# Performance work log

Measured on AMD Instinct MI355X. Metric: run time of the kernel, lower is better.

## Reference

```python
import jax, jax.numpy as jnp
import numpy as np
from jax import lax

B, C, H, W = 32, 512, 32, 32
NH = 8
ER = 4
DK_RATIO = 0.2
EPS_LN = 1e-6


def _layernorm(t, g, b):
    m = t.mean(-1, keepdims=True)
    v = ((t - m) ** 2).mean(-1, keepdims=True)
    return (t - m) / jnp.sqrt(v + EPS_LN) * g + b


def setup_inputs() -> dict:
    key = jax.random.key(0)
    ks = jax.random.split(key, 24)
    s = 0.02
    dh = C // NH
    return {
        "x": jax.random.normal(ks[0], (B, C, H, W), jnp.float32),
        "mask_u": jax.random.uniform(ks[1], (B, NH, dh, dh), jnp.float32),
        "dw_w": jax.random.normal(ks[2], (C, 1, 3, 3), jnp.float32) * s,
        "dw_b": jnp.zeros((C,), jnp.float32),
        "ln1_g": jnp.ones((C,), jnp.float32),
        "ln1_b": jnp.zeros((C,), jnp.float32),
        "qkv_w": jax.random.normal(ks[3], (3 * C, C), jnp.float32) * s,
        "qkv_b": jnp.zeros((3 * C,), jnp.float32),
        "temp": jnp.ones((NH, 1, 1), jnp.float32),
        "proj_w": jax.random.normal(ks[4], (C, C), jnp.float32) * s,
        "proj_b": jnp.zeros((C,), jnp.float32),
        "ct_w": jax.random.normal(ks[5], (C, C, 2, 2), jnp.float32) * s,  # [in,out,kH,kW]
        "ct_b": jnp.zeros((C,), jnp.float32),
        "ln2_g": jnp.ones((C,), jnp.float32),
        "ln2_b": jnp.zeros((C,), jnp.float32),
        "pw1_w": jax.random.normal(ks[6], (ER * C, C), jnp.float32) * s,
        "pw1_b": jnp.zeros((ER * C,), jnp.float32),
        "pw2_w": jax.random.normal(ks[7], (C, ER * C), jnp.float32) * s,
        "pw2_b": jnp.zeros((C,), jnp.float32),
    }


def reference(x, mask_u, dw_w, dw_b, ln1_g, ln1_b, qkv_w, qkv_b, temp,
              proj_w, proj_b, ct_w, ct_b, ln2_g, ln2_b,
              pw1_w, pw1_b, pw2_w, pw2_b):
    inp = x
    b, c, h, w = x.shape
    # depthwise 3x3 conv + residual
    dw = lax.conv_general_dilated(
        x, dw_w, (1, 1), "SAME", feature_group_count=c,
        dimension_numbers=("NCHW", "OIHW", "NCHW")) + dw_b[None, :, None, None]
    x = dw + inp
    # 2x2 avg pool, stride 2
    hp, wp = h // 2, w // 2
    x = x.reshape(b, c, hp, 2, wp, 2).mean(axis=(3, 5))  # [B,C,hp,wp]
    n = hp * wp
    # tokens [B,N,C] -> LN -> qkv
    t = x.reshape(b, c, n).transpose(0, 2, 1)
    t = _layernorm(t, ln1_g, ln1_b)
    qkv = t @ qkv_w.T + qkv_b                       # [B,N,3C]
    dh = c // NH
    qkv = qkv.reshape(b, n, 3, NH, dh).transpose(2, 0, 3, 1, 4)  # [3,B,h,N,d]
    # cosine (XCA-style) attention: transpose to [B,h,d,N], normalize over N
    q = jnp.swapaxes(qkv[0], -2, -1)
    k = jnp.swapaxes(qkv[1], -2, -1)
    v = jnp.swapaxes(qkv[2], -2, -1)
    q = q / jnp.maximum(jnp.linalg.norm(q, axis=-1, keepdims=True), 1e-12)
    k = k / jnp.maximum(jnp.linalg.norm(k, axis=-1, keepdims=True), 1e-12)
    attn = jnp.einsum("bhdn,bhen->bhde", q, k) * temp  # [B,h,d,d]
    attn = attn + (mask_u < DK_RATIO).astype(attn.dtype) * (-1e12)
    attn = jax.nn.softmax(attn, axis=-1)
    out = jnp.einsum("bhde,bhen->bhdn", attn, v)       # [B,h,d,N]
    out = out.transpose(0, 3, 1, 2).reshape(b, n, c)
    t = out @ proj_w.T + proj_b
    t = t + t
    x = t.transpose(0, 2, 1).reshape(b, c, hp, wp)
    # ConvTranspose2d(C,C,2,stride=2): each pixel expands to 2x2 block
    x = jnp.einsum("bchw,copq->bohpwq", x, ct_w).reshape(b, c, 2 * hp, 2 * wp)
    x = x + ct_b[None, :, None, None]
    # MLP in channels-last
    y = x.transpose(0, 2, 3, 1)                        # [B,H,W,C]
    y = _layernorm(y, ln2_g, ln2_b)
    y = jax.nn.gelu(y @ pw1_w.T + pw1_b, approximate=False)
    y = y @ pw2_w.T + pw2_b
    x = y.transpose(0, 3, 1, 2)
    return inp + x
```

## Files before the change

### kernel.cpp

```cpp
#include <hip/hip_runtime.h>
#include <hip/hip_bf16.h>
#include <math.h>

typedef unsigned short ushort;
typedef __attribute__((ext_vector_type(8))) short short8;
typedef __attribute__((ext_vector_type(8))) unsigned short ushort8;
typedef __attribute__((ext_vector_type(4))) unsigned short ushort4v;
typedef __attribute__((ext_vector_type(4))) float f32x4;

__device__ __forceinline__ ushort f2bb(float v) {
    return __builtin_bit_cast(ushort, __float2bfloat16(v));
}
__device__ __forceinline__ float bf2f(ushort u) {
    return __bfloat162float(__builtin_bit_cast(__hip_bfloat16, u));
}
__device__ __forceinline__ void gl2lds16(const ushort* g, ushort* l) {
    __builtin_amdgcn_global_load_lds(
        (const __attribute__((address_space(1))) unsigned int*)g,
        (__attribute__((address_space(3))) unsigned int*)l, 16, 0, 0);
}


__global__ __launch_bounds__(256) void cvtw_k(const float* __restrict__ in,
                                              ushort* __restrict__ out, int n4) {
    int i = blockIdx.x * 256 + threadIdx.x;
    if (i >= n4) return;
    float4 v = ((const float4*)in)[i];
    ushort4v o;
    o.x = f2bb(v.x); o.y = f2bb(v.y); o.z = f2bb(v.z); o.w = f2bb(v.w);
    ((ushort4v*)out)[i] = o;
}

__global__ __launch_bounds__(256) void cvtt_k(const float* __restrict__ in,
                                              ushort* __restrict__ out) {
    __shared__ float tl[32][33];
    int c0 = blockIdx.y * 32, j0 = blockIdx.x * 32;
    int tr = threadIdx.x >> 5, tc = threadIdx.x & 31;
#pragma unroll
    for (int p4 = 0; p4 < 4; ++p4)
        tl[tr + p4 * 8][tc] = in[(size_t)(c0 + tr + p4 * 8) * 2048 + j0 + tc];
    __syncthreads();
#pragma unroll
    for (int p4 = 0; p4 < 4; ++p4)
        out[(size_t)(j0 + tr + p4 * 8) * 512 + c0 + tc] = f2bb(tl[tc][tr + p4 * 8]);
}

__global__ __launch_bounds__(256) void dwpool_k(const float* __restrict__ x,
                                                const float* __restrict__ dww,
                                                const float* __restrict__ dwb,
                                                ushort* __restrict__ xp) {
    int bc = blockIdx.x;
    int c = bc & 511;
    __shared__ float tile[32][33];
    __shared__ float w9[9];
    const float* xb = x + (size_t)bc * 1024;
    int tid = threadIdx.x;
    for (int i = tid; i < 1024; i += 256) tile[i >> 5][i & 31] = xb[i];
    if (tid < 9) w9[tid] = dww[c * 9 + tid];
    __syncthreads();
    float bv = dwb[c];
    int ph = tid >> 4, pw = tid & 15;
    float s = 0.f;
#pragma unroll
    for (int dy = 0; dy < 2; ++dy) {
#pragma unroll
        for (int dx = 0; dx < 2; ++dx) {
            int hh = 2 * ph + dy, ww = 2 * pw + dx;
            float a = bv + tile[hh][ww];
#pragma unroll
            for (int ky = 0; ky < 3; ++ky) {
                int yy = hh + ky - 1;
                if (yy < 0 || yy > 31) continue;
#pragma unroll
                for (int kx = 0; kx < 3; ++kx) {
                    int xx = ww + kx - 1;
                    if (xx < 0 || xx > 31) continue;
                    a += w9[ky * 3 + kx] * tile[yy][xx];
                }
            }
            s += a;
        }
    }
    xp[(size_t)bc * 256 + tid] = f2bb(0.25f * s);
}

__global__ __launch_bounds__(256) void ln1_stats_k(const ushort* __restrict__ xp,
                                                   float* __restrict__ m1,
                                                   float* __restrict__ r1) {
    __shared__ float sh_s[4][64], sh_q[4][64];
    int blk = blockIdx.x;
    int b = blk >> 2;
    int n0 = (blk & 3) * 64;
    int t = threadIdx.x & 63, w = threadIdx.x >> 6;
    float s = 0.f, ss = 0.f;
    for (int i = 0; i < 128; ++i) {
        int c = w * 128 + i;
        float v = bf2f(xp[(size_t)(b * 512 + c) * 256 + n0 + t]);
        s += v; ss += v * v;
    }
    sh_s[w][t] = s; sh_q[w][t] = ss;
    __syncthreads();
    if (w == 0) {
        s  = sh_s[0][t] + sh_s[1][t] + sh_s[2][t] + sh_s[3][t];
        ss = sh_q[0][t] + sh_q[1][t] + sh_q[2][t] + sh_q[3][t];
        float m = s * (1.0f / 512.0f);
        m1[b * 256 + n0 + t] = m;
        r1[b * 256 + n0 + t] = rsqrtf(ss * (1.0f / 512.0f) - m * m + 1e-6f);
    }
}

__global__ __launch_bounds__(256) void ln1_apply_k(const ushort* __restrict__ xp,
                                                   const float* __restrict__ m1,
                                                   const float* __restrict__ r1,
                                                   const float* __restrict__ g,
                                                   const float* __restrict__ beta,
                                                   ushort* __restrict__ a_ln) {
    __shared__ float tl[64][66];
    int blk = blockIdx.x;
    int b = blk >> 5, ct = (blk >> 2) & 7, nt = blk & 3;
    int t = threadIdx.x;
    int rq = t >> 6, nl = t & 63;
#pragma unroll
    for (int i = 0; i < 16; ++i) {
        int r = rq * 16 + i;
        int c = ct * 64 + r;
        tl[r][nl] = bf2f(xp[(size_t)(b * 512 + c) * 256 + nt * 64 + nl]);
    }
    __syncthreads();
    int r2 = t >> 2, cq = t & 3;
    int m = b * 256 + nt * 64 + r2;
    float mu = m1[m], rs = r1[m];
#pragma unroll
    for (int hh = 0; hh < 2; ++hh) {
        ushort8 o;
#pragma unroll
        for (int j = 0; j < 8; ++j) {
            int cl = cq * 16 + hh * 8 + j;
            int c = ct * 64 + cl;
            o[j] = f2bb((tl[cl][r2] - mu) * rs * g[c] + beta[c]);
        }
        *(ushort8*)&a_ln[(size_t)m * 512 + ct * 64 + cq * 16 + hh * 8] = o;
    }
}

__global__ __launch_bounds__(256) void ln2_fuse_k(ushort* __restrict__ yB,
                                                  ushort* __restrict__ yT,
                                                  const float* __restrict__ g,
                                                  const float* __restrict__ beta) {
    int w = threadIdx.x >> 6, lane = threadIdx.x & 63;
    int row = blockIdx.x * 4 + w;
    ushort* base = (row < 8192) ? (yB + (size_t)row * 512)
                                : (yT + (size_t)(row - 8192) * 512);
    ushort8 raw = *(ushort8*)&base[lane * 8];
    float v[8];
    float s = 0.f, ss = 0.f;
#pragma unroll
    for (int j = 0; j < 8; ++j) { v[j] = bf2f(raw[j]); s += v[j]; ss += v[j] * v[j]; }
#pragma unroll
    for (int off = 1; off < 64; off <<= 1) { s += __shfl_xor(s, off); ss += __shfl_xor(ss, off); }
    float mu = s * (1.0f / 512.0f);
    float rs = rsqrtf(ss * (1.0f / 512.0f) - mu * mu + 1e-6f);
    ushort8 o;
#pragma unroll
    for (int j = 0; j < 8; ++j) {
        int c = lane * 8 + j;
        o[j] = f2bb((v[j] - mu) * rs * g[c] + beta[c]);
    }
    *(ushort8*)&base[lane * 8] = o;
}

struct GP {
    const ushort* A;
    const ushort* W;
    const float* bias;
    ushort* outB;
    ushort* outB2;
    float* outF;
    const float* inp;
    int K, m0;
};

template <int MODE, int BN>
__global__ __launch_bounds__(256) void mgemm_k(GP p) {
    constexpr int MT = (BN == 128) ? 4 : 2;
    constexpr int NT = 4;
    constexpr int ATILE = 128 * 32;
    constexpr int BTILE = BN * 32;
    constexpr int SMEM_US = 2 * (ATILE + BTILE);
    __shared__ __align__(16) ushort smem[SMEM_US];
    int tid = threadIdx.x;
    int lane = tid & 63, w = tid >> 6;
    int lr = lane & 15, lq = lane >> 4;
    int mwoff = (BN == 128) ? (w >> 1) * 64 : w * 32;
    int nwoff = (BN == 128) ? (w & 1) * 64 : 0;
    int gx = gridDim.x;
    int wgid = blockIdx.y * gx + blockIdx.x;
    int cpx = (gx * gridDim.y) >> 3;
    int swz = (wgid & 7) * cpx + (wgid >> 3);
    int bx = swz % gx, by = swz / gx;
    int mbase = by * 128, nbase = bx * BN;
    int lsub = lane >> 2;
    int cchunk = (lane & 3) ^ ((lsub >> 1) & 3);
    int lcol = cchunk * 8;
    int physc = lq ^ ((lr >> 1) & 3);
    f32x4 acc[MT][NT] = {};

    auto stage = [&](int buf, int kb) {
        ushort* Ab = smem + buf * ATILE;
        ushort* Bb = smem + 2 * ATILE + buf * BTILE;
#pragma unroll
        for (int i = 0; i < 2; ++i) {
            int row = w * 32 + i * 16;
            gl2lds16(p.A + (size_t)(mbase + row + lsub) * p.K + kb + lcol,
                     &Ab[row * 32]);
        }
        if constexpr (BN == 128) {
#pragma unroll
            for (int i = 0; i < 2; ++i) {
                int row = w * 32 + i * 16;
                gl2lds16(p.W + (size_t)(nbase + row + lsub) * p.K + kb + lcol,
                         &Bb[row * 32]);
            }
        } else {
            int row = w * 16;
            gl2lds16(p.W + (size_t)(nbase + row + lsub) * p.K + kb + lcol,
                     &Bb[row * 32]);
        }
    };

    stage(0, 0);
    __syncthreads();
    int nk = p.K >> 5;
    for (int t = 0; t < nk; ++t) {
        int cur = t & 1;
        if (t + 1 < nk) stage(cur ^ 1, (t + 1) << 5);
        const ushort* Ac = smem + cur * ATILE;
        const ushort* Bc = smem + 2 * ATILE + cur * BTILE;
        short8 af[MT], bfr[NT];
#pragma unroll
        for (int tt = 0; tt < MT; ++tt)
            af[tt] = *(const short8*)&Ac[(mwoff + tt * 16 + lr) * 32 + physc * 8];
#pragma unroll
        for (int tt = 0; tt < NT; ++tt)
            bfr[tt] = *(const short8*)&Bc[(nwoff + tt * 16 + lr) * 32 + physc * 8];
#pragma unroll
        for (int i = 0; i < MT; ++i)
#pragma unroll
            for (int j = 0; j < NT; ++j)
                acc[i][j] = __builtin_amdgcn_mfma_f32_16x16x32_bf16(af[i], bfr[j], acc[i][j], 0, 0, 0);
        __syncthreads();
    }

    if constexpr (MODE == 1 || MODE == 3) {
        const size_t LD = (MODE == 1) ? 512 : 2048;
        ushort* eb = (ushort*)smem;
#pragma unroll
        for (int h = 0; h < 2; ++h) {
            __syncthreads();
            if ((w & 1) == h) {
#pragma unroll
                for (int ti = 0; ti < MT; ++ti)
#pragma unroll
                    for (int tj = 0; tj < NT; ++tj)
#pragma unroll
                        for (int r = 0; r < 4; ++r) {
                            int row = mwoff + ti * 16 + lq * 4 + r;
                            int colh = tj * 16 + lr;
                            float v = acc[ti][tj][r] + p.bias[nbase + h * 64 + colh];
                            if constexpr (MODE == 1) v *= 2.0f;
                            else v = 0.5f * v * (1.0f + erff(v * 0.70710678118654752f));
                            int ph = (colh >> 3) ^ (row & 7);
                            eb[row * 64 + ph * 8 + (colh & 7)] = f2bb(v);
                        }
            }
            __syncthreads();
#pragma unroll
            for (int i = 0; i < 4; ++i) {
                int row = i * 32 + (tid >> 3);
                int ch = tid & 7;
                int pch = ch ^ (row & 7);
                short8 d = *(short8*)&eb[row * 64 + pch * 8];
                *(short8*)&p.outB[(size_t)(mbase + row) * LD + nbase + h * 64 + ch * 8] = d;
            }
        }
    } else if constexpr (MODE == 0) {
        ushort* eb = (ushort*)smem;
        int b = mbase >> 8, n0 = mbase & 255;
#pragma unroll
        for (int pc = 0; pc < 4; ++pc) {
            __syncthreads();
            if ((w & 1) == (pc >> 1)) {
                int tjb = (pc & 1) * 2;
#pragma unroll
                for (int ti = 0; ti < MT; ++ti)
#pragma unroll
                    for (int tj2 = 0; tj2 < 2; ++tj2)
#pragma unroll
                        for (int r = 0; r < 4; ++r) {
                            int tj = tjb + tj2;
                            int row = mwoff + ti * 16 + lq * 4 + r;
                            int cl = tj2 * 16 + lr;
                            float v = acc[ti][tj][r] + p.bias[nbase + pc * 32 + cl];
                            eb[cl * 136 + row] = f2bb(v);
                        }
            }
            __syncthreads();
#pragma unroll
            for (int i = 0; i < 2; ++i) {
                int dl = (tid >> 4) + 16 * i;
                int ch = tid & 15;
                short8 d = *(short8*)&eb[dl * 136 + ch * 8];
                int cg = nbase + pc * 32 + dl;
                int sect = cg >> 9, hh = (cg >> 6) & 7, dd = cg & 63;
                size_t addr = ((size_t)(sect * 256 + b * 8 + hh) * 64 + dd) * 256 + n0 + ch * 8;
                *(short8*)&p.outB[addr] = d;
            }
        }
    } else if constexpr (MODE == 2) {
        ushort* eb = (ushort*)smem;
        ushort* ybase = (mbase < 2048) ? p.outB : (p.outB2 - (size_t)8192 * 512);
        int obase = nbase >> 2;
#pragma unroll
        for (int hf = 0; hf < 2; ++hf) {
            __syncthreads();
            if ((w >> 1) == hf) {
#pragma unroll
                for (int ti = 0; ti < MT; ++ti)
#pragma unroll
                    for (int tj = 0; tj < NT; ++tj)
#pragma unroll
                        for (int r = 0; r < 4; ++r) {
                            int rl = (mwoff - hf * 64) + ti * 16 + lq * 4 + r;
                            int cgl = nwoff + tj * 16 + lr;
                            int o_l = cgl >> 2, pp = (cgl >> 1) & 1, qq = cgl & 1;
                            int pix = ((rl >> 4) * 2 + pp) * 32 + (rl & 15) * 2 + qq;
                            float v = acc[ti][tj][r] + p.bias[obase + o_l];
                            eb[pix * 40 + o_l] = f2bb(v);
                        }
            }
            __syncthreads();
            int hhbase = ((mbase & 255) >> 4) + hf * 4;
            int prb = (mbase >> 8) * 32 + 2 * hhbase;
#pragma unroll
            for (int i = 0; i < 4; ++i) {
                int pix = i * 64 + (tid >> 2);
                int ch = tid & 3;
                short8 d = *(short8*)&eb[pix * 40 + ch * 8];
                int pr = (prb + (pix >> 5)) * 32 + (pix & 31);
                *(short8*)&ybase[(size_t)pr * 512 + obase + ch * 8] = d;
            }
        }
    } else {
        float* ef = (float*)smem;
        int gm0 = p.m0 + mbase;
        int b = gm0 >> 10, hw0 = gm0 & 1023;
#pragma unroll
        for (int pc = 0; pc < 2; ++pc) {
            __syncthreads();
#pragma unroll
            for (int ti = 0; ti < MT; ++ti)
#pragma unroll
                for (int tj2 = 0; tj2 < 2; ++tj2)
#pragma unroll
                    for (int r = 0; r < 4; ++r) {
                        int tj = pc * 2 + tj2;
                        int row = mwoff + ti * 16 + lq * 4 + r;
                        int cl = tj2 * 16 + lr;
                        ef[cl * 132 + row] = acc[ti][tj][r] + p.bias[nbase + pc * 32 + cl];
                    }
            __syncthreads();
#pragma unroll
            for (int i = 0; i < 4; ++i) {
                int cl = (tid >> 5) + 8 * i;
                int ck = tid & 31;
                float4 v4 = *(float4*)&ef[cl * 132 + ck * 4];
                int c = nbase + pc * 32 + cl;
                size_t idx = ((size_t)(b * 512 + c)) * 1024 + hw0 + ck * 4;
                float4 xin = *(const float4*)&p.inp[idx];
                float4 o4;
                o4.x = xin.x + v4.x; o4.y = xin.y + v4.y;
                o4.z = xin.z + v4.z; o4.w = xin.w + v4.w;
                *(float4*)&p.outF[idx] = o4;
            }
        }
    }
}

__global__ __launch_bounds__(256) void attn_k(const ushort* __restrict__ qkvp,
                                              const float* __restrict__ mask_u,
                                              const float* __restrict__ temp,
                                              ushort* __restrict__ attn_out) {
    __shared__ float bufA[64 * 65];
    __shared__ float bufB[64 * 65];
    __shared__ float Sb[64 * 65];
    __shared__ float fq[64], fk[64];
    int tid = threadIdx.x;
    int bh = blockIdx.x;
    int b = bh >> 3, h = bh & 7;
    const ushort* q = qkvp + (size_t)bh * 16384;
    const ushort* k = qkvp + 4194304 + (size_t)bh * 16384;
    const ushort* v = qkvp + 8388608 + (size_t)bh * 16384;
    int wv = tid >> 6, lane = tid & 63;

    for (int rr = 0; rr < 16; ++rr) {
        int row = wv * 16 + rr;
        float s = 0.f;
#pragma unroll
        for (int i = 0; i < 4; ++i) { float xv = bf2f(q[row * 256 + lane + i * 64]); s += xv * xv; }
#pragma unroll
        for (int off = 32; off; off >>= 1) s += __shfl_down(s, off);
        if (lane == 0) fq[row] = 1.0f / fmaxf(sqrtf(s), 1e-12f);
        s = 0.f;
#pragma unroll
        for (int i = 0; i < 4; ++i) { float xv = bf2f(k[row * 256 + lane + i * 64]); s += xv * xv; }
#pragma unroll
        for (int off = 32; off; off >>= 1) s += __shfl_down(s, off);
        if (lane == 0) fk[row] = 1.0f / fmaxf(sqrtf(s), 1e-12f);
    }
    __syncthreads();

    int tx = tid & 15, ty = tid >> 4;
    float acc[4][4] = {};
    for (int nb = 0; nb < 256; nb += 64) {
        __syncthreads();
#pragma unroll
        for (int it = 0; it < 16; ++it) {
            int f = it * 256 + tid;
            int d = f >> 6, n = f & 63;
            bufA[d * 65 + n] = bf2f(q[d * 256 + nb + n]);
            bufB[d * 65 + n] = bf2f(k[d * 256 + nb + n]);
        }
        __syncthreads();
#pragma unroll 8
        for (int kk = 0; kk < 64; ++kk) {
            float a[4], bb[4];
#pragma unroll
            for (int i = 0; i < 4; ++i) a[i] = bufA[(ty * 4 + i) * 65 + kk];
#pragma unroll
            for (int j = 0; j < 4; ++j) bb[j] = bufB[(tx * 4 + j) * 65 + kk];
#pragma unroll
            for (int i = 0; i < 4; ++i)
#pragma unroll
                for (int j = 0; j < 4; ++j) acc[i][j] += a[i] * bb[j];
        }
    }
    float tv = temp[h];
    __syncthreads();
#pragma unroll
    for (int i = 0; i < 4; ++i) {
        int d = ty * 4 + i;
#pragma unroll
        for (int j = 0; j < 4; ++j) {
            int e = tx * 4 + j;
            float sc = acc[i][j] * fq[d] * fk[e] * tv;
            float mu = mask_u[((size_t)bh * 64 + d) * 64 + e];
            if (mu < 0.2f) sc -= 1e12f;
            Sb[d * 65 + e] = sc;
        }
    }
    __syncthreads();

    {
        int row = tid >> 2, sub = tid & 3;
        float ev[16];
        float mx = -INFINITY;
#pragma unroll
        for (int i = 0; i < 16; ++i) { float s = Sb[row * 65 + sub * 16 + i]; ev[i] = s; mx = fmaxf(mx, s); }
        mx = fmaxf(mx, __shfl_xor(mx, 1));
        mx = fmaxf(mx, __shfl_xor(mx, 2));
        float sum = 0.f;
#pragma unroll
        for (int i = 0; i < 16; ++i) { ev[i] = expf(ev[i] - mx); sum += ev[i]; }
        sum += __shfl_xor(sum, 1);
        sum += __shfl_xor(sum, 2);
        float inv = 1.0f / sum;
#pragma unroll
        for (int i = 0; i < 16; ++i) Sb[row * 65 + sub * 16 + i] = ev[i] * inv;
    }
    __syncthreads();

    for (int nb = 0; nb < 256; nb += 64) {
        __syncthreads();
#pragma unroll
        for (int it = 0; it < 16; ++it) {
            int f = it * 256 + tid;
            int e = f >> 6, n = f & 63;
            bufA[e * 65 + n] = bf2f(v[e * 256 + nb + n]);
        }
        __syncthreads();
        float o[4][4] = {};
#pragma unroll 8
        for (int kk = 0; kk < 64; ++kk) {
            float a[4], bb[4];
#pragma unroll
            for (int i = 0; i < 4; ++i) a[i] = Sb[(ty * 4 + i) * 65 + kk];
#pragma unroll
            for (int j = 0; j < 4; ++j) bb[j] = bufA[kk * 65 + tx * 4 + j];
#pragma unroll
            for (int i = 0; i < 4; ++i)
#pragma unroll
                for (int j = 0; j < 4; ++j) o[i][j] += a[i] * bb[j];
        }
#pragma unroll
        for (int j = 0; j < 4; ++j) {
            int n = nb + tx * 4 + j;
            size_t base = ((size_t)(b * 256 + n)) * 512 + h * 64 + ty * 4;
#pragma unroll
            for (int i = 0; i < 4; ++i) attn_out[base + i] = f2bb(o[i][j]);
        }
    }
}

extern "C" void kernel_launch(void* const* d_in, const int* in_sizes, int n_in,
                              void* d_out, int out_size, void* d_ws, size_t ws_size,
                              hipStream_t stream) {
    const float* x      = (const float*)d_in[0];
    const float* mask_u = (const float*)d_in[1];
    const float* dw_w   = (const float*)d_in[2];
    const float* dw_b   = (const float*)d_in[3];
    const float* ln1_g  = (const float*)d_in[4];
    const float* ln1_b  = (const float*)d_in[5];
    const float* qkv_w  = (const float*)d_in[6];
    const float* qkv_b  = (const float*)d_in[7];
    const float* temp   = (const float*)d_in[8];
    const float* proj_w = (const float*)d_in[9];
    const float* proj_b = (const float*)d_in[10];
    const float* ct_w   = (const float*)d_in[11];
    const float* ct_b   = (const float*)d_in[12];
    const float* ln2_g  = (const float*)d_in[13];
    const float* ln2_b  = (const float*)d_in[14];
    const float* pw1_w  = (const float*)d_in[15];
    const float* pw1_b  = (const float*)d_in[16];
    const float* pw2_w  = (const float*)d_in[17];
    const float* pw2_b  = (const float*)d_in[18];

    char* wsb = (char*)d_ws;
    float* mean1 = (float*)wsb;
    float* rstd1 = mean1 + 8192;
    ushort* wq = (ushort*)(wsb + 524288);
    ushort* wp = wq + 786432;
    ushort* wc = wp + 262144;
    ushort* w1 = wc + 1048576;
    ushort* w2 = w1 + 1048576;
    ushort* xp     = (ushort*)(wsb + 8912896);
    ushort* t2     = xp;
    ushort* a_ln   = (ushort*)(wsb + 17301504);
    ushort* yB     = a_ln;
    ushort* qkvp   = (ushort*)(wsb + 25690112);
    ushort* attn_o = (ushort*)(wsb + 50855936);
    ushort* h1c    = qkvp;
    ushort* yT     = (ushort*)(wsb + 59244544);

    cvtw_k<<<768,  256, 0, stream>>>(qkv_w,  wq, 196608);
    cvtw_k<<<256,  256, 0, stream>>>(proj_w, wp, 65536);
    cvtw_k<<<1024, 256, 0, stream>>>(pw1_w,  w1, 262144);
    cvtw_k<<<1024, 256, 0, stream>>>(pw2_w,  w2, 262144);
    cvtt_k<<<dim3(64, 16), 256, 0, stream>>>(ct_w, wc);
    dwpool_k<<<32 * 512, 256, 0, stream>>>(x, dw_w, dw_b, xp);
    ln1_stats_k<<<128, 256, 0, stream>>>(xp, mean1, rstd1);
    ln1_apply_k<<<1024, 256, 0, stream>>>(xp, mean1, rstd1, ln1_g, ln1_b, a_ln);
    {
        GP p{}; p.A = a_ln; p.W = wq; p.bias = qkv_b; p.outB = qkvp; p.K = 512;
        mgemm_k<0, 128><<<dim3(12, 64), 256, 0, stream>>>(p);
    }
    attn_k<<<256, 256, 0, stream>>>(qkvp, mask_u, temp, attn_o);
    {
        GP p{}; p.A = attn_o; p.W = wp; p.bias = proj_b; p.outB = t2; p.K = 512;
        mgemm_k<1, 128><<<dim3(4, 64), 256, 0, stream>>>(p);
    }
    {
        GP p{}; p.A = t2; p.W = wc; p.bias = ct_b;
        p.outB = yB; p.outB2 = yT; p.K = 512;
        mgemm_k<2, 128><<<dim3(16, 64), 256, 0, stream>>>(p);
    }
    ln2_fuse_k<<<8192, 256, 0, stream>>>(yB, yT, ln2_g, ln2_b);
    for (int c = 0; c < 4; ++c) {
        int m0 = c * 8192;
        const ushort* yChunk = (c == 0) ? yB : (yT + (size_t)(m0 - 8192) * 512);
        {
            GP p{}; p.A = yChunk; p.W = w1; p.bias = pw1_b; p.outB = h1c; p.K = 512;
            mgemm_k<3, 128><<<dim3(16, 64), 256, 0, stream>>>(p);
        }
        {
            GP p{}; p.A = h1c; p.W = w2; p.bias = pw2_b;
            p.outF = (float*)d_out; p.inp = x; p.K = 2048; p.m0 = m0;
            mgemm_k<4, 64><<<dim3(8, 64), 256, 0, stream>>>(p);
        }
    }
}
```

Before: 671.5 us.

## Use MFMA for channel attention and store V transposed from QKV GEMM

The attention kernel's two scalar-FMA matmuls (q·kᵀ over N and softmax·V) become bf16 MFMA 16x16x32 instructions. Fragments load straight from global memory, and the softmax probabilities go to LDS as bf16 in a swizzled layout. To make V contiguous along the reduction dimension, the QKV GEMM epilogue now writes the V section transposed ([bh][n][d]). The output stores are also vectorized. Rounding P to bf16 adds some precision loss, and the transposed V write uses a strided gather from LDS.

```diff
diff --git a/kernel.cpp b/kernel.cpp
--- a/kernel.cpp
+++ b/kernel.cpp
@@ -305,15 +305,31 @@
                         }
             }
             __syncthreads();
-#pragma unroll
-            for (int i = 0; i < 2; ++i) {
-                int dl = (tid >> 4) + 16 * i;
-                int ch = tid & 15;
-                short8 d = *(short8*)&eb[dl * 136 + ch * 8];
-                int cg = nbase + pc * 32 + dl;
-                int sect = cg >> 9, hh = (cg >> 6) & 7, dd = cg & 63;
-                size_t addr = ((size_t)(sect * 256 + b * 8 + hh) * 64 + dd) * 256 + n0 + ch * 8;
-                *(short8*)&p.outB[addr] = d;
+            if (nbase < 1024) {
+#pragma unroll
+                for (int i = 0; i < 2; ++i) {
+                    int dl = (tid >> 4) + 16 * i;
+                    int ch = tid & 15;
+                    short8 d = *(short8*)&eb[dl * 136 + ch * 8];
+                    int cg = nbase + pc * 32 + dl;
+                    int sect = cg >> 9, hh = (cg >> 6) & 7, dd = cg & 63;
+                    size_t addr = ((size_t)(sect * 256 + b * 8 + hh) * 64 + dd) * 256 + n0 + ch * 8;
+                    *(short8*)&p.outB[addr] = d;
+                }
+            } else {
+                int cv = nbase + pc * 32 - 1024;
+                int bh2 = b * 8 + (cv >> 6);
+                int d0 = cv & 63;
+#pragma unroll
+                for (int i = 0; i < 2; ++i) {
+                    int idx = i * 256 + tid;
+                    int n = idx >> 2, oc = idx & 3;
+                    ushort8 dv;
+#pragma unroll
+                    for (int j = 0; j < 8; ++j) dv[j] = eb[(oc * 8 + j) * 136 + n];
+                    *(ushort8*)&p.outB[(size_t)8388608 + (size_t)bh2 * 16384 +
+                                       (size_t)(n0 + n) * 64 + d0 + oc * 8] = dv;
+                }
             }
         }
     } else if constexpr (MODE == 2) {
@@ -390,74 +406,74 @@
                                               const float* __restrict__ mask_u,
                                               const float* __restrict__ temp,
                                               ushort* __restrict__ attn_out) {
-    __shared__ float bufA[64 * 65];
-    __shared__ float bufB[64 * 65];
     __shared__ float Sb[64 * 65];
+    __shared__ ushort Pb[64 * 64];
     __shared__ float fq[64], fk[64];
     int tid = threadIdx.x;
     int bh = blockIdx.x;
     int b = bh >> 3, h = bh & 7;
-    const ushort* q = qkvp + (size_t)bh * 16384;
-    const ushort* k = qkvp + 4194304 + (size_t)bh * 16384;
-    const ushort* v = qkvp + 8388608 + (size_t)bh * 16384;
-    int wv = tid >> 6, lane = tid & 63;
-
-    for (int rr = 0; rr < 16; ++rr) {
-        int row = wv * 16 + rr;
-        float s = 0.f;
-#pragma unroll
-        for (int i = 0; i < 4; ++i) { float xv = bf2f(q[row * 256 + lane + i * 64]); s += xv * xv; }
-#pragma unroll
-        for (int off = 32; off; off >>= 1) s += __shfl_down(s, off);
-        if (lane == 0) fq[row] = 1.0f / fmaxf(sqrtf(s), 1e-12f);
-        s = 0.f;
-#pragma unroll
-        for (int i = 0; i < 4; ++i) { float xv = bf2f(k[row * 256 + lane + i * 64]); s += xv * xv; }
-#pragma unroll
-        for (int off = 32; off; off >>= 1) s += __shfl_down(s, off);
-        if (lane == 0) fk[row] = 1.0f / fmaxf(sqrtf(s), 1e-12f);
-    }
-    __syncthreads();
-
-    int tx = tid & 15, ty = tid >> 4;
-    float acc[4][4] = {};
-    for (int nb = 0; nb < 256; nb += 64) {
-        __syncthreads();
-#pragma unroll
-        for (int it = 0; it < 16; ++it) {
-            int f = it * 256 + tid;
-            int d = f >> 6, n = f & 63;
-            bufA[d * 65 + n] = bf2f(q[d * 256 + nb + n]);
-            bufB[d * 65 + n] = bf2f(k[d * 256 + nb + n]);
-        }
-        __syncthreads();
-#pragma unroll 8
-        for (int kk = 0; kk < 64; ++kk) {
-            float a[4], bb[4];
-#pragma unroll
-            for (int i = 0; i < 4; ++i) a[i] = bufA[(ty * 4 + i) * 65 + kk];
-#pragma unroll
-            for (int j = 0; j < 4; ++j) bb[j] = bufB[(tx * 4 + j) * 65 + kk];
-#pragma unroll
-            for (int i = 0; i < 4; ++i)
-#pragma unroll
-                for (int j = 0; j < 4; ++j) acc[i][j] += a[i] * bb[j];
-        }
-    }
+    const ushort* q  = qkvp + (size_t)bh * 16384;
+    const ushort* k  = qkvp + 4194304 + (size_t)bh * 16384;
+    const ushort* vt = qkvp + 8388608 + (size_t)bh * 16384;
+    int lane = tid & 63, w = tid >> 6;
+    int lr = lane & 15, lq = lane >> 4;
+
+    {
+        int row = tid >> 2, qd = tid & 3;
+        const ushort* qr = q + row * 256 + qd * 64;
+        const ushort* kr = k + row * 256 + qd * 64;
+        float s = 0.f, t = 0.f;
+#pragma unroll
+        for (int i = 0; i < 8; ++i) {
+            short8 a8 = *(const short8*)&qr[i * 8];
+            short8 b8 = *(const short8*)&kr[i * 8];
+#pragma unroll
+            for (int j = 0; j < 8; ++j) {
+                float fa = bf2f((ushort)a8[j]); s += fa * fa;
+                float fb = bf2f((ushort)b8[j]); t += fb * fb;
+            }
+        }
+        s += __shfl_xor(s, 1); s += __shfl_xor(s, 2);
+        t += __shfl_xor(t, 1); t += __shfl_xor(t, 2);
+        if (qd == 0) {
+            fq[row] = 1.0f / fmaxf(sqrtf(s), 1e-12f);
+            fk[row] = 1.0f / fmaxf(sqrtf(t), 1e-12f);
+        }
+    }
+    __syncthreads();
+
+    int mq = (w >> 1) * 32, nq = (w & 1) * 32;
+    f32x4 acc[2][2] = {};
+    for (int kb = 0; kb < 256; kb += 32) {
+        short8 af[2], bfr[2];
+#pragma unroll
+        for (int ti = 0; ti < 2; ++ti)
+            af[ti] = *(const short8*)&q[(mq + ti * 16 + lr) * 256 + kb + lq * 8];
+#pragma unroll
+        for (int tj = 0; tj < 2; ++tj)
+            bfr[tj] = *(const short8*)&k[(nq + tj * 16 + lr) * 256 + kb + lq * 8];
+#pragma unroll
+        for (int i = 0; i < 2; ++i)
+#pragma unroll
+            for (int j = 0; j < 2; ++j)
+                acc[i][j] = __builtin_amdgcn_mfma_f32_16x16x32_bf16(af[i], bfr[j], acc[i][j], 0, 0, 0);
+    }
+
     float tv = temp[h];
-    __syncthreads();
-#pragma unroll
-    for (int i = 0; i < 4; ++i) {
-        int d = ty * 4 + i;
-#pragma unroll
-        for (int j = 0; j < 4; ++j) {
-            int e = tx * 4 + j;
-            float sc = acc[i][j] * fq[d] * fk[e] * tv;
-            float mu = mask_u[((size_t)bh * 64 + d) * 64 + e];
-            if (mu < 0.2f) sc -= 1e12f;
-            Sb[d * 65 + e] = sc;
-        }
-    }
+#pragma unroll
+    for (int i = 0; i < 2; ++i)
+#pragma unroll
+        for (int r = 0; r < 4; ++r) {
+            int d = mq + i * 16 + lq * 4 + r;
+#pragma unroll
+            for (int j = 0; j < 2; ++j) {
+                int e = nq + j * 16 + lr;
+                float sc = acc[i][j][r] * fq[d] * fk[e] * tv;
+                float mu = mask_u[((size_t)bh * 64 + d) * 64 + e];
+                if (mu < 0.2f) sc -= 1e12f;
+                Sb[d * 65 + e] = sc;
+            }
+        }
     __syncthreads();
 
     {
@@ -474,39 +490,48 @@
         sum += __shfl_xor(sum, 1);
         sum += __shfl_xor(sum, 2);
         float inv = 1.0f / sum;
-#pragma unroll
-        for (int i = 0; i < 16; ++i) Sb[row * 65 + sub * 16 + i] = ev[i] * inv;
-    }
-    __syncthreads();
-
-    for (int nb = 0; nb < 256; nb += 64) {
-        __syncthreads();
-#pragma unroll
-        for (int it = 0; it < 16; ++it) {
-            int f = it * 256 + tid;
-            int e = f >> 6, n = f & 63;
-            bufA[e * 65 + n] = bf2f(v[e * 256 + nb + n]);
-        }
-        __syncthreads();
-        float o[4][4] = {};
-#pragma unroll 8
-        for (int kk = 0; kk < 64; ++kk) {
-            float a[4], bb[4];
-#pragma unroll
-            for (int i = 0; i < 4; ++i) a[i] = Sb[(ty * 4 + i) * 65 + kk];
-#pragma unroll
-            for (int j = 0; j < 4; ++j) bb[j] = bufA[kk * 65 + tx * 4 + j];
-#pragma unroll
-            for (int i = 0; i < 4; ++i)
-#pragma unroll
-                for (int j = 0; j < 4; ++j) o[i][j] += a[i] * bb[j];
-        }
-#pragma unroll
-        for (int j = 0; j < 4; ++j) {
-            int n = nb + tx * 4 + j;
-            size_t base = ((size_t)(b * 256 + n)) * 512 + h * 64 + ty * 4;
-#pragma unroll
-            for (int i = 0; i < 4; ++i) attn_out[base + i] = f2bb(o[i][j]);
+        unsigned int* Pb32 = (unsigned int*)Pb;
+#pragma unroll
+        for (int kk = 0; kk < 8; ++kk) {
+            unsigned int lo = f2bb(ev[2 * kk] * inv);
+            unsigned int hi = f2bb(ev[2 * kk + 1] * inv);
+            int c8 = sub * 2 + (kk >> 2);
+            int ph = c8 ^ (row & 7);
+            Pb32[row * 32 + ph * 4 + (kk & 3)] = (hi << 16) | lo;
+        }
+    }
+    __syncthreads();
+
+    int nw = w * 64;
+    f32x4 o[4][4] = {};
+#pragma unroll
+    for (int ks = 0; ks < 2; ++ks) {
+        short8 pa[4];
+#pragma unroll
+        for (int mt = 0; mt < 4; ++mt) {
+            int d = mt * 16 + lr;
+            int ph = (ks * 4 + lq) ^ (d & 7);
+            pa[mt] = *(const short8*)&Pb[d * 64 + ph * 8];
+        }
+#pragma unroll
+        for (int nt = 0; nt < 4; ++nt) {
+            short8 vb = *(const short8*)&vt[(size_t)(nw + nt * 16 + lr) * 64 + ks * 32 + lq * 8];
+#pragma unroll
+            for (int mt = 0; mt < 4; ++mt)
+                o[mt][nt] = __builtin_amdgcn_mfma_f32_16x16x32_bf16(pa[mt], vb, o[mt][nt], 0, 0, 0);
+        }
+    }
+
+#pragma unroll
+    for (int mt = 0; mt < 4; ++mt) {
+        int d0 = mt * 16 + lq * 4;
+#pragma unroll
+        for (int nt = 0; nt < 4; ++nt) {
+            int n = nw + nt * 16 + lr;
+            ushort4v ov;
+#pragma unroll
+            for (int r = 0; r < 4; ++r) ov[r] = f2bb(o[mt][nt][r]);
+            *(ushort4v*)&attn_out[((size_t)(b * 256 + n)) * 512 + h * 64 + d0] = ov;
         }
     }
 }
```

Result: faster. 619.1 us (-7.8%).
